# Performance work log

Hardware: AMD Instinct MI355X
Metric: run time of the kernel (lower is better)

The kernel has to match this reference:

```python
import jax, jax.numpy as jnp
import numpy as np

N = 20000; E = 160000; C = 64; SH = 9; NB = 8
S_DIM = 16; MS_HID = 64; FC_HID = 64
RATE = 0.1; LAMBDA = 0.5; R_MAX = 5.0; EV_PER = 16
K = int(RATE * N)          # static master-node count (top-k selection)
E_V = EV_PER * K           # static virtual-edge budget


def _safe_len(vec):
    # smooth norm, safe under autodiff at zero-length edges (self loops)
    return jnp.sqrt(jnp.sum(vec * vec, axis=-1, keepdims=True) + 1e-12)


def _sh(vec):
    # real spherical harmonics lmax=2, 'component' normalization, on unit vectors
    n = vec / _safe_len(vec)
    x, y, z = n[:, 0], n[:, 1], n[:, 2]
    s3 = jnp.sqrt(3.0); s15 = jnp.sqrt(15.0); s5 = jnp.sqrt(5.0)
    return jnp.stack([
        jnp.ones_like(x),
        s3 * x, s3 * y, s3 * z,
        s15 * x * y, s15 * y * z, 0.5 * s5 * (3 * z * z - 1.0),
        s15 * x * z, 0.5 * s15 * (x * x - y * y),
    ], axis=-1)  # [E, 9]


def _bessel(r):
    # Bessel radial basis with p=6 polynomial cutoff envelope; r: [E,1]
    n = jnp.arange(1, NB + 1, dtype=r.dtype)
    b = jnp.sqrt(2.0 / R_MAX) * jnp.sin(n * jnp.pi * r / R_MAX) / jnp.clip(r, 1e-9)
    u = jnp.clip(r / R_MAX, 0.0, 1.0); p = 6.0
    env = 1.0 - (p + 1) * (p + 2) / 2 * u ** p + p * (p + 2) * u ** (p + 1) - p * (p + 1) / 2 * u ** (p + 2)
    return b * env  # [E, NB]


def _conv(h, src, dst, sh, ef, emask, n_nodes, fc_w1, fc_b1, fc_w2, fc_b2, lin_w):
    # TFN-style tensor-product conv: per-edge weights from radial MLP,
    # message = flatten(h[dst] outer sh) * w -> linear -> scatter-mean to src
    w = jax.nn.relu(ef @ fc_w1 + fc_b1) @ fc_w2 + fc_b2            # [E, C*SH]
    tp = (h[dst][:, :, None] * sh[:, None, :]).reshape(sh.shape[0], -1) * w
    msg = (tp @ lin_w) * emask[:, None]                            # [E, C]
    agg = jax.ops.segment_sum(msg, src, num_segments=n_nodes)
    deg = jax.ops.segment_sum(emask, src, num_segments=n_nodes)
    return agg / jnp.clip(deg, 1.0)[:, None]


def setup_inputs() -> dict:
    key = jax.random.key(0)
    ks = jax.random.split(key, 12)
    def lin(k, i, o):
        return (jax.random.normal(k, (i, o), jnp.float32) / np.sqrt(i)).astype(jnp.float32)
    return {
        "h": jax.random.normal(ks[0], (N, C), jnp.float32),
        "pos": jax.random.uniform(ks[1], (N, 3), jnp.float32) * 10.0,
        "edge_index": jax.random.randint(ks[2], (2, E), 0, N, dtype=jnp.int32),
        "fc_w1": lin(ks[3], NB, FC_HID), "fc_b1": jnp.zeros((FC_HID,), jnp.float32),
        "fc_w2": lin(ks[4], FC_HID, C * SH), "fc_b2": jnp.zeros((C * SH,), jnp.float32),
        "lin_w": lin(ks[5], C * SH, C),
        "ms_w1": lin(ks[6], S_DIM, MS_HID), "ms_b1": jnp.zeros((MS_HID,), jnp.float32),
        "ms_w2": lin(ks[7], MS_HID, 1), "ms_b2": jnp.zeros((1,), jnp.float32),
        "vg_wq": lin(ks[8], S_DIM, S_DIM), "vg_wk": lin(ks[9], S_DIM, S_DIM),
    }


def reference(h, pos, fc_w1, fc_b1, fc_w2, fc_b2, lin_w,
              ms_w1, ms_b1, ms_w2, ms_b2, vg_wq, vg_wk, edge_index):
    src, dst = edge_index[0], edge_index[1]
    vec = pos[src] - pos[dst]
    sh = _sh(vec)
    ef = _bessel(_safe_len(vec))
    ones_e = jnp.ones((E,), h.dtype)
    h_update = _conv(h, src, dst, sh, ef, ones_e, N, fc_w1, fc_b1, fc_w2, fc_b2, lin_w)
    h_local = h_update + h  # in_dim == out_dim -> pad is a no-op

    # --- master selection (top-k by learned score; static K) ---
    h_sc = h_local[:, :S_DIM]
    score = jax.nn.sigmoid(
        (jax.nn.relu(h_sc @ ms_w1 + ms_b1) @ ms_w2 + ms_b2).squeeze(-1))  # [N]
    _, top_idx = jax.lax.top_k(score, K)
    node_mask = jnp.zeros((N,), h.dtype).at[top_idx].set(1.0)
    m = score * node_mask
    master_idx = jnp.sort(top_idx)

    # relabel full-graph ids -> master-subgraph ids (masked subgraph extraction)
    node2m = jnp.full((N,), -1, jnp.int32).at[master_idx].set(jnp.arange(K, dtype=jnp.int32))
    src_m, dst_m = node2m[src], node2m[dst]
    e_mask = ((src_m >= 0) & (dst_m >= 0)).astype(h.dtype)
    src_mc = jnp.where(src_m >= 0, src_m, 0)
    dst_mc = jnp.where(dst_m >= 0, dst_m, 0)
    adj = jnp.zeros((K, K), h.dtype).at[src_mc, dst_mc].add(e_mask)

    h_master = h_local[master_idx]
    pos_master = pos[master_idx]
    h_ms = h_master[:, :S_DIM]

    # --- virtual edge generation (attention, thresholded by lambda) ---
    q = h_ms @ vg_wq; kk = h_ms @ vg_wk
    attn = jax.nn.sigmoid(q @ kk.T / np.sqrt(S_DIM))  # [K, K]
    exist = (adj > 0) | jnp.eye(K, dtype=bool)
    A_virtual = jnp.where((~exist) & (attn > LAMBDA), 1.0, 0.0).astype(h.dtype)
    vvals, vidx = jax.lax.top_k((attn * A_virtual).reshape(-1), E_V)
    v_src = (vidx // K).astype(jnp.int32); v_dst = (vidx % K).astype(jnp.int32)
    v_mask = (vvals > 0).astype(h.dtype)

    src_all = jnp.concatenate([src_mc, v_src])
    dst_all = jnp.concatenate([dst_mc, v_dst])
    mask_all = jnp.concatenate([e_mask, v_mask])
    vec_m = pos_master[src_all] - pos_master[dst_all]
    sh_m = _sh(vec_m)
    ef_m = _bessel(_safe_len(vec_m))
    h_m_update = _conv(h_master, src_all, dst_all, sh_m, ef_m, mask_all, K,
                       fc_w1, fc_b1, fc_w2, fc_b2, lin_w)
    h_hier = h_m_update + h_master

    h_hier_exp = jnp.zeros_like(h_local).at[master_idx].set(h_hier)
    m_e = m[:, None]
    h_final = (1.0 - m_e) * h_local + m_e * h_hier_exp
    return (h_final, pos, A_virtual, m)
```

## Files before the change

kernel.cpp:

```cpp
#include <hip/hip_runtime.h>
#include <stdint.h>

constexpr int N_   = 20000;
constexpr int E_   = 160000;
constexpr int C_   = 64;
constexpr int K_   = 2000;
constexpr int EV_  = 32000;
constexpr int EALL_ = E_ + EV_;
constexpr int CSH_ = 576;
constexpr int TB_  = 64;

constexpr size_t OFF_AGG    = 0;
constexpr size_t OFF_DEG    = 5120000;
constexpr size_t OFF_AGGM   = 5200000;
constexpr size_t OFF_DEGM   = 5712000;
constexpr size_t OFF_RANK   = 5720000;
constexpr size_t OFF_MASKA  = 5800000;
constexpr size_t OFF_EXIST  = 6568000;
constexpr size_t OFF_HIST   = 10568000;
constexpr size_t OFF_STATE  = 10572096;
constexpr size_t ZERO_BYTES = 10572352;
constexpr size_t OFF_HLOCAL = 10572352;
constexpr size_t OFF_KEY    = 15692352;
constexpr size_t OFF_SCORE  = 15852352;
constexpr size_t OFF_N2M    = 15932352;
constexpr size_t OFF_MIDX   = 16012352;
constexpr size_t OFF_HM     = 16020352;
constexpr size_t OFF_POSM   = 16532352;
constexpr size_t OFF_Q      = 16556352;
constexpr size_t OFF_KBUF   = 16684352;
constexpr size_t OFF_SRCA   = 16812352;
constexpr size_t OFF_DSTA   = 17580352;
constexpr size_t OFF_TMAX   = 18348352;
constexpr size_t OFF_CAND   = 18410880;

struct RState {
    unsigned long long prefix;
    int R;
    unsigned int cand_count;
    unsigned int sel_count;
    int bin_thresh;
    unsigned int total;
    unsigned int pad;
};

__global__ void k_w0(const float* __restrict__ fc_b1, const float* __restrict__ fc_w2,
                     const float* __restrict__ fc_b2, int* __restrict__ w0nz)
{
    __shared__ float hid0[64];
    __shared__ int nz;
    int tid = threadIdx.x;
    if (tid == 0) nz = 0;
    if (tid < 64) hid0[tid] = fmaxf(fc_b1[tid], 0.0f);
    __syncthreads();
    if (tid < CSH_) {
        float acc = fc_b2[tid];
        for (int k = 0; k < 64; k++) acc += hid0[k] * fc_w2[k * CSH_ + tid];
        if (acc != 0.0f) atomicOr(&nz, 1);
    }
    __syncthreads();
    if (tid == 0) *w0nz = nz;
}

__global__ __launch_bounds__(256) void k_prep(
    int n_edges, const int* __restrict__ src, const int* __restrict__ dst,
    const float* __restrict__ mask, const float* __restrict__ posn,
    const int* __restrict__ w0nz, float* __restrict__ deg,
    float* __restrict__ edata, unsigned int* __restrict__ cnt)
{
    int e = blockIdx.x * 256 + threadIdx.x;
    bool valid = e < n_edges;
    int s_i = 0, d_i = 0; float msk = 0.0f;
    if (valid) {
        msk = mask ? mask[e] : 1.0f;
        if (msk != 0.0f) { s_i = src[e]; d_i = dst[e]; }
    }
    bool active = valid && (msk != 0.0f);

    float vx = 0.f, vy = 0.f, vz = 0.f;
    if (active) {
        vx = posn[s_i*3+0] - posn[d_i*3+0];
        vy = posn[s_i*3+1] - posn[d_i*3+1];
        vz = posn[s_i*3+2] - posn[d_i*3+2];
    }
    float r = sqrtf(vx*vx + vy*vy + vz*vz + 1e-12f);
    float invr = 1.0f / r;
    float x = vx*invr, y = vy*invr, z = vz*invr;
    const float s3 = 1.7320508075688772f, s15 = 3.872983346207417f, s5 = 2.23606797749979f;
    float sh[9];
    sh[0] = 1.0f; sh[1] = s3*x; sh[2] = s3*y; sh[3] = s3*z;
    sh[4] = s15*x*y; sh[5] = s15*y*z; sh[6] = 0.5f*s5*(3.0f*z*z - 1.0f);
    sh[7] = s15*x*z; sh[8] = 0.5f*s15*(x*x - y*y);

    float u = r * 0.2f; u = u > 1.0f ? 1.0f : u;
    float u2 = u*u, u6 = u2*u2*u2, u7 = u6*u, u8 = u7*u;
    float env = 1.0f - 28.0f*u6 + 48.0f*u7 - 21.0f*u8;
    float rc = r > 1e-9f ? r : 1e-9f;
    const float bpref = 0.6324555320336759f;
    const float PIov5 = 0.6283185307179586f;
    float ef[8];
    #pragma unroll
    for (int n = 0; n < 8; n++)
        ef[n] = bpref * sinf(PIov5 * r * (float)(n + 1)) / rc * env;

    if (active) atomicAdd(&deg[s_i], msk);

    bool contrib = active && !((env == 0.0f) && (*w0nz == 0));
    int lane = threadIdx.x & 63;
    unsigned long long b = __ballot(contrib);
    int wc = __popcll(b);
    int base = 0;
    if (lane == 0 && wc) base = (int)atomicAdd(cnt, (unsigned)wc);
    base = __shfl(base, 0);
    if (contrib) {
        int slot = base + __popcll(b & ((1ull << lane) - 1ull));
        float* p = edata + (size_t)slot * 20;
        #pragma unroll
        for (int n = 0; n < 8; n++) p[n] = ef[n];
        #pragma unroll
        for (int t = 0; t < 9; t++) p[8+t] = sh[t];
        p[17] = __int_as_float(s_i);
        p[18] = __int_as_float(d_i);
        p[19] = msk;
    }
}

__global__ __launch_bounds__(256, 3) void k_convg(
    const unsigned int* __restrict__ cnt, const float* __restrict__ edata,
    const float* __restrict__ hn,
    const float* __restrict__ fc_w1, const float* __restrict__ fc_b1,
    const float* __restrict__ fc_w2, const float* __restrict__ fc_b2,
    const float* __restrict__ lin_w, float* __restrict__ agg)
{
    __shared__ float s_misc[TB_ * 12];
    __shared__ __align__(16) float s_hid[64 * 64];
    __shared__ __align__(16) float s_tp[64 * 68];
    __shared__ __align__(16) float s_w[4096];

    const int tid = threadIdx.x;
    const int oq = (tid & 15) * 4;
    const int e0 = (tid >> 4) * 4;

    const int nheavy = (int)*cnt;
    const int nblk = (nheavy + TB_ - 1) / TB_;

    for (int blk = blockIdx.x; blk < nblk; blk += gridDim.x) {
        const int ebase = blk * TB_;
        int nE = nheavy - ebase; if (nE > TB_) nE = TB_;

        __syncthreads();
        for (int idx = tid; idx < TB_ * 12; idx += 256) {
            int e = idx / 12, f = idx - 12 * e;
            float v = 0.0f;
            if (e < nE) {
                const float* p = edata + (size_t)(ebase + e) * 20;
                v = (f < 9) ? p[8 + f] : (f == 9) ? p[17] : (f == 10) ? p[19] : p[18];
            }
            s_misc[idx] = v;
        }
        for (int idx = tid; idx < TB_ * 64; idx += 256) {
            int k = idx >> 6, e = idx & 63;
            float hv = 0.0f;
            if (e < nE) {
                const float* p = edata + (size_t)(ebase + e) * 20;
                float acc = fc_b1[k];
                #pragma unroll
                for (int n = 0; n < 8; n++) acc += p[n] * fc_w1[n * 64 + k];
                hv = fmaxf(acc, 0.0f);
            }
            s_hid[k * 64 + e] = hv;
        }
        float acc[4][4] = {{0,0,0,0},{0,0,0,0},{0,0,0,0},{0,0,0,0}};
        __syncthreads();

        const int d0 = __float_as_int(s_misc[(e0+0) * 12 + 11]);
        const int d1 = __float_as_int(s_misc[(e0+1) * 12 + 11]);
        const int d2 = __float_as_int(s_misc[(e0+2) * 12 + 11]);
        const int d3 = __float_as_int(s_misc[(e0+3) * 12 + 11]);

        for (int cj = 0; cj < 9; cj++) {
            const int j0 = cj * 64;
            if (cj) __syncthreads();
            for (int i4 = tid; i4 < 1024; i4 += 256) {
                int k = i4 >> 4, q4 = (i4 & 15) * 4;
                *reinterpret_cast<float4*>(&s_w[k * 64 + q4]) =
                    *reinterpret_cast<const float4*>(&fc_w2[k * CSH_ + j0 + q4]);
            }
            __syncthreads();

            const int jb = j0 + oq;
            const int c0 = jb / 9, c1 = (jb + 3) / 9;
            float hA0 = hn[d0 * 64 + c0], hB0 = hn[d0 * 64 + c1];
            float hA1 = hn[d1 * 64 + c0], hB1 = hn[d1 * 64 + c1];
            float hA2 = hn[d2 * 64 + c0], hB2 = hn[d2 * 64 + c1];
            float hA3 = hn[d3 * 64 + c0], hB3 = hn[d3 * 64 + c1];

            float a[4][4];
            #pragma unroll
            for (int q = 0; q < 4; q++) {
                float b = fc_b2[jb + q];
                a[0][q]=b; a[1][q]=b; a[2][q]=b; a[3][q]=b;
            }
            #pragma unroll 4
            for (int k = 0; k < 64; k++) {
                float4 w4 = *reinterpret_cast<const float4*>(&s_w[k * 64 + oq]);
                float4 h4 = *reinterpret_cast<const float4*>(&s_hid[k * 64 + e0]);
                a[0][0]+=h4.x*w4.x; a[0][1]+=h4.x*w4.y; a[0][2]+=h4.x*w4.z; a[0][3]+=h4.x*w4.w;
                a[1][0]+=h4.y*w4.x; a[1][1]+=h4.y*w4.y; a[1][2]+=h4.y*w4.z; a[1][3]+=h4.y*w4.w;
                a[2][0]+=h4.z*w4.x; a[2][1]+=h4.z*w4.y; a[2][2]+=h4.z*w4.z; a[2][3]+=h4.z*w4.w;
                a[3][0]+=h4.w*w4.x; a[3][1]+=h4.w*w4.y; a[3][2]+=h4.w*w4.z; a[3][3]+=h4.w*w4.w;
            }
            #pragma unroll
            for (int q = 0; q < 4; q++) {
                int j = jb + q; int cc = j / 9; int si = j - 9 * cc;
                float4 tpv;
                tpv.x = (cc == c0 ? hA0 : hB0) * s_misc[(e0+0) * 12 + si] * a[0][q];
                tpv.y = (cc == c0 ? hA1 : hB1) * s_misc[(e0+1) * 12 + si] * a[1][q];
                tpv.z = (cc == c0 ? hA2 : hB2) * s_misc[(e0+2) * 12 + si] * a[2][q];
                tpv.w = (cc == c0 ? hA3 : hB3) * s_misc[(e0+3) * 12 + si] * a[3][q];
                *reinterpret_cast<float4*>(&s_tp[(oq + q) * 68 + e0]) = tpv;
            }
            __syncthreads();

            for (int i4 = tid; i4 < 1024; i4 += 256) {
                *reinterpret_cast<float4*>(&s_w[i4 * 4]) =
                    *reinterpret_cast<const float4*>(&lin_w[j0 * 64 + i4 * 4]);
            }
            __syncthreads();

            #pragma unroll 4
            for (int jj = 0; jj < 64; jj++) {
                float4 l4 = *reinterpret_cast<const float4*>(&s_w[jj * 64 + oq]);
                float4 t4 = *reinterpret_cast<const float4*>(&s_tp[jj * 68 + e0]);
                acc[0][0]+=t4.x*l4.x; acc[0][1]+=t4.x*l4.y; acc[0][2]+=t4.x*l4.z; acc[0][3]+=t4.x*l4.w;
                acc[1][0]+=t4.y*l4.x; acc[1][1]+=t4.y*l4.y; acc[1][2]+=t4.y*l4.z; acc[1][3]+=t4.y*l4.w;
                acc[2][0]+=t4.z*l4.x; acc[2][1]+=t4.z*l4.y; acc[2][2]+=t4.z*l4.z; acc[2][3]+=t4.z*l4.w;
                acc[3][0]+=t4.w*l4.x; acc[3][1]+=t4.w*l4.y; acc[3][2]+=t4.w*l4.z; acc[3][3]+=t4.w*l4.w;
            }
        }

        #pragma unroll
        for (int t = 0; t < 4; t++) {
            float mk = s_misc[(e0+t) * 12 + 10];
            if (mk != 0.0f) {
                int s = __float_as_int(s_misc[(e0+t) * 12 + 9]);
                #pragma unroll
                for (int q = 0; q < 4; q++) atomicAdd(&agg[s * 64 + oq + q], acc[t][q] * mk);
            }
        }
    }
}

__global__ __launch_bounds__(256) void k_hlscore(const float* __restrict__ h,
    const float* __restrict__ agg, const float* __restrict__ deg,
    const float* __restrict__ ms_w1, const float* __restrict__ ms_b1,
    const float* __restrict__ ms_w2, const float* __restrict__ ms_b2,
    float* __restrict__ h_local, float* __restrict__ score, unsigned long long* __restrict__ key)
{
    int wid = threadIdx.x >> 6, lane = threadIdx.x & 63;
    int n = blockIdx.x * 4 + wid;
    if (n >= N_) return;
    float d = fmaxf(deg[n], 1.0f);
    float hl = h[n*64 + lane] + agg[n*64 + lane] / d;
    h_local[n*64 + lane] = hl;
    float acc = ms_b1[lane];
    #pragma unroll
    for (int i = 0; i < 16; i++) acc += __shfl(hl, i) * ms_w1[i*64 + lane];
    acc = fmaxf(acc, 0.0f);
    float part = acc * ms_w2[lane];
    #pragma unroll
    for (int off = 32; off > 0; off >>= 1) part += __shfl_xor(part, off);
    if (lane == 0) {
        float s = part + ms_b2[0];
        float sc = 1.0f / (1.0f + expf(-s));
        score[n] = sc;
        key[n] = ((unsigned long long)__float_as_uint(sc) << 32)
               | (unsigned long long)(0xFFFFFFFFu - (unsigned)n);
    }
}

__global__ __launch_bounds__(256) void k_rank(const unsigned long long* __restrict__ key,
                                              int* __restrict__ rankcnt)
{
    int i = blockIdx.x * 256 + threadIdx.x;
    int seg = blockIdx.y;
    int lo = seg * 1250, hi = lo + 1250;
    unsigned long long my = (i < N_) ? key[i] : ~0ull;
    int cnt = 0;
    #pragma unroll 8
    for (int j = lo; j < hi; j++) cnt += (key[j] > my) ? 1 : 0;
    if (i < N_ && cnt) atomicAdd(&rankcnt[i], cnt);
}

__global__ __launch_bounds__(1024) void k_scanfin(const int* __restrict__ rankcnt,
    const float* __restrict__ score, int* __restrict__ node2m, int* __restrict__ midx,
    float* __restrict__ m_out)
{
    __shared__ int wsum[16];
    __shared__ int wbase[16];
    __shared__ int s_base;
    int tid = threadIdx.x, lane = tid & 63, wv = tid >> 6;
    if (tid == 0) s_base = 0;
    __syncthreads();
    for (int c = 0; c < 20; c++) {
        int idx = c * 1024 + tid;
        int sel = 0;
        if (idx < N_) {
            sel = (rankcnt[idx] < K_) ? 1 : 0;
            m_out[idx] = sel ? score[idx] : 0.0f;
        }
        int v = sel;
        #pragma unroll
        for (int off = 1; off < 64; off <<= 1) {
            int u = __shfl_up(v, off);
            if (lane >= off) v += u;
        }
        if (lane == 63) wsum[wv] = v;
        __syncthreads();
        if (tid == 0) {
            int runb = s_base;
            for (int w = 0; w < 16; w++) { wbase[w] = runb; runb += wsum[w]; }
            s_base = runb;
        }
        __syncthreads();
        if (idx < N_) {
            if (sel) { int rk = wbase[wv] + v - 1; node2m[idx] = rk; midx[rk] = idx; }
            else node2m[idx] = -1;
        }
    }
}

__global__ __launch_bounds__(256) void k_mastex(const int* __restrict__ midx,
    const float* __restrict__ h_local, const float* __restrict__ pos,
    const float* __restrict__ vg_wq, const float* __restrict__ vg_wk,
    const int* __restrict__ src, const int* __restrict__ dst, const int* __restrict__ node2m,
    float* __restrict__ h_m, float* __restrict__ pos_m,
    float* __restrict__ qbuf, float* __restrict__ kbuf,
    int* __restrict__ src_all, int* __restrict__ dst_all,
    float* __restrict__ mask_all, unsigned char* __restrict__ exist)
{
    int b = blockIdx.x;
    if (b < 500) {
        int mi = b * 4 + (threadIdx.x >> 6);
        int lane = threadIdx.x & 63;
        int node = midx[mi];
        h_m[mi*64 + lane] = h_local[node*64 + lane];
        if (lane < 3) pos_m[mi*3 + lane] = pos[node*3 + lane];
        if (lane < 32) {
            int j = lane & 15;
            const float* wm = (lane < 16) ? vg_wq : vg_wk;
            float acc = 0.0f;
            #pragma unroll
            for (int i = 0; i < 16; i++) acc += h_local[node*64 + i] * wm[i*16 + j];
            if (lane < 16) qbuf[mi*16 + j] = acc; else kbuf[mi*16 + j] = acc;
        }
    } else {
        int e = (b - 500) * 256 + threadIdx.x;
        int sm = node2m[src[e]], dm = node2m[dst[e]];
        bool em = (sm >= 0) && (dm >= 0);
        int smc = sm >= 0 ? sm : 0;
        int dmc = dm >= 0 ? dm : 0;
        src_all[e] = smc; dst_all[e] = dmc; mask_all[e] = em ? 1.0f : 0.0f;
        if (em) exist[smc * K_ + dmc] = 1;
    }
}

constexpr int NTILE_ = (K_ / 16) * (K_ / 16);
__global__ __launch_bounds__(256) void k_attn1(const float* __restrict__ qbuf,
    const float* __restrict__ kbuf, const unsigned char* __restrict__ exist,
    float* __restrict__ Av, float* __restrict__ tmax, unsigned int* __restrict__ hist,
    RState* st, unsigned int* __restrict__ done_ctr)
{
    constexpr int TBK = K_ / 16;
    __shared__ float sq[16][17], sk[16][17];
    __shared__ unsigned int lh[1024];
    __shared__ float wmax[4];
    __shared__ unsigned int ha[1024], hb[1024];
    __shared__ unsigned int s_last;
    int tid = threadIdx.x;
    for (int b = tid; b < 1024; b += 256) lh[b] = 0;

    for (int t = blockIdx.x; t < NTILE_; t += gridDim.x) {
        int bi = t / TBK, bj = t % TBK;
        int i0 = bi * 16, j0 = bj * 16;
        int r = tid >> 4, c = tid & 15;
        __syncthreads();
        sq[r][c] = qbuf[(i0 + r) * 16 + c];
        sk[r][c] = kbuf[(j0 + r) * 16 + c];
        __syncthreads();
        int ti = tid >> 4, tj = tid & 15;
        float dot = 0.0f;
        #pragma unroll
        for (int cc = 0; cc < 16; cc++) dot += sq[ti][cc] * sk[tj][cc];
        float attn = 1.0f / (1.0f + expf(-dot * 0.25f));
        int gi = i0 + ti, gj = j0 + tj;
        int flat = gi * K_ + gj;
        bool ex = (exist[flat] != 0) || (gi == gj);
        bool av = (!ex) && (attn > 0.5f);
        Av[flat] = av ? 1.0f : 0.0f;
        float cv = av ? attn : 0.0f;
        if (av) {
            unsigned bin = (__float_as_uint(attn) - 0x3F000000u) >> 13;
            if (bin > 1023u) bin = 1023u;
            atomicAdd(&lh[bin], 1u);
        }
        float wm = cv;
        #pragma unroll
        for (int off = 32; off > 0; off >>= 1) wm = fmaxf(wm, __shfl_xor(wm, off));
        int wid = tid >> 6, lane = tid & 63;
        if (lane == 0) wmax[wid] = wm;
        __syncthreads();
        if (tid == 0) tmax[t] = fmaxf(fmaxf(wmax[0], wmax[1]), fmaxf(wmax[2], wmax[3]));
    }
    __syncthreads();
    for (int b = tid; b < 1024; b += 256) {
        unsigned v = lh[b];
        if (v) atomicAdd(&hist[b], v);
    }
    __syncthreads();
    __threadfence();
    if (tid == 0) s_last = (atomicAdd(done_ctr, 1u) == (unsigned)gridDim.x - 1u) ? 1u : 0u;
    __syncthreads();
    if (!s_last) return;
    __threadfence();
    for (int b = tid; b < 1024; b += 256) ha[b] = hist[b];
    __syncthreads();
    unsigned* srcp = ha; unsigned* dstp = hb;
    for (int off = 1; off < 1024; off <<= 1) {
        for (int b = tid; b < 1024; b += 256)
            dstp[b] = srcp[b] + ((b + off < 1024) ? srcp[b + off] : 0u);
        __syncthreads();
        unsigned* tmp = srcp; srcp = dstp; dstp = tmp;
    }
    unsigned total = srcp[0];
    int R = (total < (unsigned)EV_) ? (int)total : EV_;
    if (tid == 0) {
        st->R = R; st->total = total; st->cand_count = 0; st->sel_count = 0;
        if (R == 0) st->bin_thresh = 1024;
    }
    __syncthreads();
    if (R > 0) {
        for (int b = tid; b < 1024; b += 256) {
            unsigned hi2 = (b == 1023) ? 0u : srcp[b + 1];
            if ((int)srcp[b] >= R && (int)hi2 < R) st->bin_thresh = b;
        }
    }
}

__global__ __launch_bounds__(256) void k_attn2(const float* __restrict__ qbuf,
    const float* __restrict__ kbuf, const unsigned char* __restrict__ exist,
    const float* __restrict__ tmax, RState* st, unsigned long long* __restrict__ cand)
{
    constexpr int TBK = K_ / 16;
    __shared__ float sq[16][17], sk[16][17];
    __shared__ int wb[4];
    __shared__ int bb;
    int tid = threadIdx.x;
    unsigned tbits = 0x3F000000u + ((unsigned)st->bin_thresh << 13);

    for (int t = blockIdx.x; t < NTILE_; t += gridDim.x) {
        if (__float_as_uint(tmax[t]) < tbits) continue;
        int bi = t / TBK, bj = t % TBK;
        int i0 = bi * 16, j0 = bj * 16;
        int r = tid >> 4, c = tid & 15;
        __syncthreads();
        sq[r][c] = qbuf[(i0 + r) * 16 + c];
        sk[r][c] = kbuf[(j0 + r) * 16 + c];
        __syncthreads();
        int ti = tid >> 4, tj = tid & 15;
        float dot = 0.0f;
        #pragma unroll
        for (int cc = 0; cc < 16; cc++) dot += sq[ti][cc] * sk[tj][cc];
        float attn = 1.0f / (1.0f + expf(-dot * 0.25f));
        int gi = i0 + ti, gj = j0 + tj;
        int flat = gi * K_ + gj;
        bool ex = (exist[flat] != 0) || (gi == gj);
        bool store = (!ex) && (attn > 0.5f) && (__float_as_uint(attn) >= tbits);

        unsigned long long keyv = ((unsigned long long)__float_as_uint(attn) << 32)
                                | (unsigned long long)(0xFFFFFFFFu - (unsigned)flat);
        int wid = tid >> 6, lane = tid & 63;
        unsigned long long b = __ballot(store);
        int wc = __popcll(b);
        if (lane == 0) wb[wid] = wc;
        __syncthreads();
        if (tid == 0) {
            int s = 0;
            for (int w = 0; w < 4; w++) { int cc2 = wb[w]; wb[w] = s; s += cc2; }
            bb = s ? (int)atomicAdd(&st->cand_count, (unsigned)s) : 0;
        }
        __syncthreads();
        if (store) {
            int slot = bb + wb[wid] + __popcll(b & ((1ull << lane) - 1ull));
            cand[slot] = keyv;
        }
    }
}

__global__ __launch_bounds__(1024) void k_radixsel(RState* st,
    const unsigned long long* __restrict__ cand,
    int* __restrict__ src_all, int* __restrict__ dst_all, float* __restrict__ mask_all)
{
    __shared__ unsigned int lh[256];
    __shared__ unsigned int suf[256];
    __shared__ unsigned int s_tie[8192];
    __shared__ unsigned int s_pref, s_R, s_tiecnt, s_cfth;
    int tid = threadIdx.x;
    int n = (int)st->cand_count;
    int R = st->R;
    if (tid == 0) { s_pref = 0x3F000000u; s_R = (unsigned)R; s_tiecnt = 0; s_cfth = 0; }
    __syncthreads();

    unsigned long long T;
    if (R > 0) {
        for (int p = 0; p < 3; p++) {
            if (tid < 256) lh[tid] = 0;
            __syncthreads();
            unsigned pref = s_pref;
            int sh_d = 16 - 8 * p;
            unsigned pm = 0xFFFFFFFFu << (sh_d + 8);
            for (int i = tid; i < n; i += 1024) {
                unsigned a = (unsigned)(cand[i] >> 32);
                if ((a & pm) == (pref & pm))
                    atomicAdd(&lh[(a >> sh_d) & 255u], 1u);
            }
            __syncthreads();
            if (tid < 256) suf[tid] = lh[tid];
            __syncthreads();
            for (int off = 1; off < 256; off <<= 1) {
                unsigned v = 0;
                if (tid < 256 && tid + off < 256) v = suf[tid + off];
                __syncthreads();
                if (tid < 256) suf[tid] += v;
                __syncthreads();
            }
            if (tid < 256) {
                unsigned Rc = s_R;
                unsigned hi2 = (tid == 255) ? 0u : suf[tid + 1];
                if (suf[tid] >= Rc && hi2 < Rc) {
                    s_pref = pref | ((unsigned)tid << sh_d);
                    s_R = Rc - hi2;
                }
            }
            __syncthreads();
        }
        unsigned Ta = s_pref;
        unsigned Rrem = s_R;
        for (int i = tid; i < n; i += 1024) {
            unsigned long long kv = cand[i];
            if ((unsigned)(kv >> 32) == Ta) {
                unsigned pos = atomicAdd(&s_tiecnt, 1u);
                if (pos < 8192u) s_tie[pos] = (unsigned)(kv & 0xFFFFFFFFull);
            }
        }
        __syncthreads();
        unsigned Cq = s_tiecnt; if (Cq > 8192u) Cq = 8192u;
        if (Rrem >= 1u && Rrem < Cq) {
            for (int i = tid; i < (int)Cq; i += 1024) {
                unsigned me = s_tie[i];
                unsigned r = 0;
                for (int j = 0; j < (int)Cq; j++) r += (s_tie[j] > me) ? 1u : 0u;
                if (r == Rrem - 1u) s_cfth = me;
            }
        }
        __syncthreads();
        T = ((unsigned long long)Ta << 32) | (unsigned long long)s_cfth;
    } else {
        T = ~0ull;
    }

    int lane = tid & 63;
    for (int i0 = 0; i0 < n; i0 += 1024) {
        int i = i0 + tid;
        bool sel = (i < n) && (cand[i] >= T);
        unsigned long long b = __ballot(sel);
        int wc = __popcll(b);
        int basep = 0;
        if (lane == 0 && wc) basep = (int)atomicAdd(&st->sel_count, (unsigned)wc);
        basep = __shfl(basep, 0);
        if (sel) {
            int slot = basep + __popcll(b & ((1ull << lane) - 1ull));
            if (slot < EV_) {
                unsigned flat = 0xFFFFFFFFu - (unsigned)(cand[i] & 0xFFFFFFFFull);
                src_all[E_ + slot] = (int)(flat / (unsigned)K_);
                dst_all[E_ + slot] = (int)(flat % (unsigned)K_);
                mask_all[E_ + slot] = 1.0f;
            }
        }
    }
}

__global__ void k_finalpos(const float* __restrict__ h_local, const int* __restrict__ node2m,
    const float* __restrict__ aggm, const float* __restrict__ degm, const float* __restrict__ h_m,
    const float* __restrict__ m_out, const float* __restrict__ pos,
    float* __restrict__ out_h, float* __restrict__ out_pos)
{
    int idx = blockIdx.x * 256 + threadIdx.x;
    if (idx < N_ * 3) out_pos[idx] = pos[idx];
    if (idx >= N_ * C_) return;
    int i = idx >> 6, c = idx & 63;
    float mval = m_out[i];
    int mi = node2m[i];
    float hh = 0.0f;
    if (mi >= 0) hh = aggm[mi*64 + c] / fmaxf(degm[mi], 1.0f) + h_m[mi*64 + c];
    out_h[idx] = (1.0f - mval) * h_local[idx] + mval * hh;
}

extern "C" void kernel_launch(void* const* d_in, const int* in_sizes, int n_in,
                              void* d_out, int out_size, void* d_ws, size_t ws_size,
                              hipStream_t stream)
{
    (void)in_sizes; (void)n_in; (void)out_size; (void)ws_size;
    const float* h     = (const float*)d_in[0];
    const float* pos   = (const float*)d_in[1];
    const int*   eidx  = (const int*)d_in[2];
    const float* fc_w1 = (const float*)d_in[3];
    const float* fc_b1 = (const float*)d_in[4];
    const float* fc_w2 = (const float*)d_in[5];
    const float* fc_b2 = (const float*)d_in[6];
    const float* lin_w = (const float*)d_in[7];
    const float* ms_w1 = (const float*)d_in[8];
    const float* ms_b1 = (const float*)d_in[9];
    const float* ms_w2 = (const float*)d_in[10];
    const float* ms_b2 = (const float*)d_in[11];
    const float* vg_wq = (const float*)d_in[12];
    const float* vg_wk = (const float*)d_in[13];

    char* ws = (char*)d_ws;
    float* agg     = (float*)(ws + OFF_AGG);
    float* deg     = (float*)(ws + OFF_DEG);
    float* aggm    = (float*)(ws + OFF_AGGM);
    float* degm    = (float*)(ws + OFF_DEGM);
    int*   rankcnt = (int*)(ws + OFF_RANK);
    float* mask_all = (float*)(ws + OFF_MASKA);
    unsigned char* exist = (unsigned char*)(ws + OFF_EXIST);
    unsigned int* hist = (unsigned int*)(ws + OFF_HIST);
    RState* st     = (RState*)(ws + OFF_STATE);
    unsigned int* cnt0 = (unsigned int*)(ws + OFF_STATE + 64);
    unsigned int* cnt1 = (unsigned int*)(ws + OFF_STATE + 68);
    int*   w0nz    = (int*)(ws + OFF_STATE + 72);
    unsigned int* done_a1 = (unsigned int*)(ws + OFF_STATE + 76);
    float* h_local = (float*)(ws + OFF_HLOCAL);
    unsigned long long* key = (unsigned long long*)(ws + OFF_KEY);
    float* score   = (float*)(ws + OFF_SCORE);
    int*   node2m  = (int*)(ws + OFF_N2M);
    int*   midx    = (int*)(ws + OFF_MIDX);
    float* h_m     = (float*)(ws + OFF_HM);
    float* pos_m   = (float*)(ws + OFF_POSM);
    float* qbuf    = (float*)(ws + OFF_Q);
    float* kbuf    = (float*)(ws + OFF_KBUF);
    int*   src_all = (int*)(ws + OFF_SRCA);
    int*   dst_all = (int*)(ws + OFF_DSTA);
    float* tmax    = (float*)(ws + OFF_TMAX);
    unsigned long long* cand = (unsigned long long*)(ws + OFF_CAND);
    float* edata   = (float*)(ws + OFF_CAND);

    float* out_h   = (float*)d_out;
    float* out_pos = out_h + (size_t)N_ * C_;
    float* out_av  = out_pos + (size_t)N_ * 3;
    float* out_m   = out_av + (size_t)K_ * K_;

    hipMemsetAsync(ws, 0, ZERO_BYTES, stream);

    k_w0<<<1, 576, 0, stream>>>(fc_b1, fc_w2, fc_b2, w0nz);

    k_prep<<<E_ / 256, 256, 0, stream>>>(E_, eidx, eidx + E_, nullptr, pos, w0nz, deg, edata, cnt0);
    k_convg<<<768, 256, 0, stream>>>(cnt0, edata, h, fc_w1, fc_b1, fc_w2, fc_b2, lin_w, agg);

    k_hlscore<<<(N_ + 3) / 4, 256, 0, stream>>>(h, agg, deg, ms_w1, ms_b1, ms_w2, ms_b2,
                                                h_local, score, key);

    k_rank<<<dim3((N_ + 255) / 256, 16), 256, 0, stream>>>(key, rankcnt);
    k_scanfin<<<1, 1024, 0, stream>>>(rankcnt, score, node2m, midx, out_m);

    k_mastex<<<500 + E_ / 256, 256, 0, stream>>>(midx, h_local, pos, vg_wq, vg_wk,
        eidx, eidx + E_, node2m, h_m, pos_m, qbuf, kbuf, src_all, dst_all, mask_all, exist);

    k_attn1<<<1024, 256, 0, stream>>>(qbuf, kbuf, exist, out_av, tmax, hist, st, done_a1);
    k_attn2<<<1024, 256, 0, stream>>>(qbuf, kbuf, exist, tmax, st, cand);
    k_radixsel<<<1, 1024, 0, stream>>>(st, cand, src_all, dst_all, mask_all);

    k_prep<<<EALL_ / 256, 256, 0, stream>>>(EALL_, src_all, dst_all, mask_all, pos_m, w0nz,
                                            degm, edata, cnt1);
    k_convg<<<768, 256, 0, stream>>>(cnt1, edata, h_m, fc_w1, fc_b1, fc_w2, fc_b2, lin_w, aggm);

    k_finalpos<<<(N_ * C_ + 255) / 256, 256, 0, stream>>>(h_local, node2m, aggm, degm, h_m,
                                                          out_m, pos, out_h, out_pos);
}
```

Measured before the change: 737.8 us.

## Fuse workspace zeroing into init kernel and merge rank with scan via last-block

```diff
diff --git a/kernel.cpp b/kernel.cpp
--- a/kernel.cpp
+++ b/kernel.cpp
@@ -19,7 +19,6 @@
 constexpr size_t OFF_EXIST  = 6568000;
 constexpr size_t OFF_HIST   = 10568000;
 constexpr size_t OFF_STATE  = 10572096;
-constexpr size_t ZERO_BYTES = 10572352;
 constexpr size_t OFF_HLOCAL = 10572352;
 constexpr size_t OFF_KEY    = 15692352;
 constexpr size_t OFF_SCORE  = 15852352;
@@ -44,22 +43,30 @@
     unsigned int pad;
 };
 
-__global__ void k_w0(const float* __restrict__ fc_b1, const float* __restrict__ fc_w2,
-                     const float* __restrict__ fc_b2, int* __restrict__ w0nz)
-{
-    __shared__ float hid0[64];
-    __shared__ int nz;
-    int tid = threadIdx.x;
-    if (tid == 0) nz = 0;
-    if (tid < 64) hid0[tid] = fmaxf(fc_b1[tid], 0.0f);
-    __syncthreads();
-    if (tid < CSH_) {
-        float acc = fc_b2[tid];
-        for (int k = 0; k < 64; k++) acc += hid0[k] * fc_w2[k * CSH_ + tid];
-        if (acc != 0.0f) atomicOr(&nz, 1);
-    }
-    __syncthreads();
-    if (tid == 0) *w0nz = nz;
+__global__ __launch_bounds__(256) void k_init(const float* __restrict__ fc_b1,
+    const float* __restrict__ fc_w2, const float* __restrict__ fc_b2, char* __restrict__ ws)
+{
+    float4 zero4 = make_float4(0.f, 0.f, 0.f, 0.f);
+    float4* z = (float4*)ws;
+    int nz4 = (int)(OFF_STATE / 16);
+    for (int i = blockIdx.x * 256 + threadIdx.x; i < nz4; i += gridDim.x * 256) z[i] = zero4;
+    if (blockIdx.x == gridDim.x - 1) {
+        __shared__ float hid0[64];
+        __shared__ int nz;
+        int t = threadIdx.x;
+        float4* zs = (float4*)(ws + OFF_STATE);
+        if (t < 16) zs[t] = zero4;
+        if (t == 0) nz = 0;
+        if (t < 64) hid0[t] = fmaxf(fc_b1[t], 0.0f);
+        __syncthreads();
+        for (int j = t; j < CSH_; j += 256) {
+            float acc = fc_b2[j];
+            for (int k = 0; k < 64; k++) acc += hid0[k] * fc_w2[k * CSH_ + j];
+            if (acc != 0.0f) atomicOr(&nz, 1);
+        }
+        __syncthreads();
+        if (t == 0) *(int*)(ws + OFF_STATE + 72) = nz;
+    }
 }
 
 __global__ __launch_bounds__(256) void k_prep(
@@ -279,52 +286,63 @@
     }
 }
 
-__global__ __launch_bounds__(256) void k_rank(const unsigned long long* __restrict__ key,
-                                              int* __restrict__ rankcnt)
-{
-    int i = blockIdx.x * 256 + threadIdx.x;
-    int seg = blockIdx.y;
-    int lo = seg * 1250, hi = lo + 1250;
-    unsigned long long my = (i < N_) ? key[i] : ~0ull;
-    int cnt = 0;
-    #pragma unroll 8
-    for (int j = lo; j < hi; j++) cnt += (key[j] > my) ? 1 : 0;
-    if (i < N_ && cnt) atomicAdd(&rankcnt[i], cnt);
-}
-
-__global__ __launch_bounds__(1024) void k_scanfin(const int* __restrict__ rankcnt,
-    const float* __restrict__ score, int* __restrict__ node2m, int* __restrict__ midx,
-    float* __restrict__ m_out)
-{
-    __shared__ int wsum[16];
-    __shared__ int wbase[16];
-    __shared__ int s_base;
+__global__ __launch_bounds__(256) void k_rankscan(const unsigned long long* __restrict__ key,
+    int* __restrict__ rankcnt, const float* __restrict__ score,
+    int* __restrict__ node2m, int* __restrict__ midx, float* __restrict__ m_out,
+    unsigned int* __restrict__ done)
+{
     int tid = threadIdx.x, lane = tid & 63, wv = tid >> 6;
-    if (tid == 0) s_base = 0;
-    __syncthreads();
-    for (int c = 0; c < 20; c++) {
-        int idx = c * 1024 + tid;
-        int sel = 0;
+    {
+        int ib = blockIdx.x % 79;
+        int seg = blockIdx.x / 79;
+        int i = ib * 256 + tid;
+        int lo = seg * 1250, hi = lo + 1250;
+        unsigned long long my = (i < N_) ? key[i] : ~0ull;
+        int cnt = 0;
+        #pragma unroll 8
+        for (int j = lo; j < hi; j++) cnt += (key[j] > my) ? 1 : 0;
+        if (i < N_ && cnt) atomicAdd(&rankcnt[i], cnt);
+    }
+    __threadfence();
+    __syncthreads();
+    __shared__ unsigned int s_last;
+    if (tid == 0) s_last = (atomicAdd(done, 1u) == (unsigned)gridDim.x - 1u) ? 1u : 0u;
+    __syncthreads();
+    if (!s_last) return;
+    __threadfence();
+
+    const int base = tid * 79;
+    unsigned long long m0 = 0ull; unsigned m1 = 0u;
+    int csel = 0;
+    for (int k = 0; k < 79; k++) {
+        int idx = base + k;
         if (idx < N_) {
-            sel = (rankcnt[idx] < K_) ? 1 : 0;
+            int r = atomicAdd(&rankcnt[idx], 0);
+            int sel = (r < K_) ? 1 : 0;
             m_out[idx] = sel ? score[idx] : 0.0f;
-        }
-        int v = sel;
-        #pragma unroll
-        for (int off = 1; off < 64; off <<= 1) {
-            int u = __shfl_up(v, off);
-            if (lane >= off) v += u;
-        }
-        if (lane == 63) wsum[wv] = v;
-        __syncthreads();
-        if (tid == 0) {
-            int runb = s_base;
-            for (int w = 0; w < 16; w++) { wbase[w] = runb; runb += wsum[w]; }
-            s_base = runb;
-        }
-        __syncthreads();
+            if (sel) {
+                if (k < 64) m0 |= (1ull << k); else m1 |= (1u << (k - 64));
+                csel++;
+            }
+        }
+    }
+    __shared__ int wsum[4], wbase[4];
+    int v = csel;
+    #pragma unroll
+    for (int off = 1; off < 64; off <<= 1) {
+        int u = __shfl_up(v, off);
+        if (lane >= off) v += u;
+    }
+    if (lane == 63) wsum[wv] = v;
+    __syncthreads();
+    if (tid == 0) { int run = 0; for (int w = 0; w < 4; w++) { int c = wsum[w]; wbase[w] = run; run += c; } }
+    __syncthreads();
+    int run = wbase[wv] + v - csel;
+    for (int k = 0; k < 79; k++) {
+        int idx = base + k;
         if (idx < N_) {
-            if (sel) { int rk = wbase[wv] + v - 1; node2m[idx] = rk; midx[rk] = idx; }
+            bool sel = (k < 64) ? ((m0 >> k) & 1ull) : ((m1 >> (k - 64)) & 1u);
+            if (sel) { node2m[idx] = run; midx[run] = idx; run++; }
             else node2m[idx] = -1;
         }
     }
@@ -423,7 +441,7 @@
     __syncthreads();
     if (!s_last) return;
     __threadfence();
-    for (int b = tid; b < 1024; b += 256) ha[b] = hist[b];
+    for (int b = tid; b < 1024; b += 256) ha[b] = atomicAdd(&hist[b], 0u);
     __syncthreads();
     unsigned* srcp = ha; unsigned* dstp = hb;
     for (int off = 1; off < 1024; off <<= 1) {
@@ -640,6 +658,7 @@
     unsigned int* cnt1 = (unsigned int*)(ws + OFF_STATE + 68);
     int*   w0nz    = (int*)(ws + OFF_STATE + 72);
     unsigned int* done_a1 = (unsigned int*)(ws + OFF_STATE + 76);
+    unsigned int* done_rk = (unsigned int*)(ws + OFF_STATE + 80);
     float* h_local = (float*)(ws + OFF_HLOCAL);
     unsigned long long* key = (unsigned long long*)(ws + OFF_KEY);
     float* score   = (float*)(ws + OFF_SCORE);
@@ -660,9 +679,7 @@
     float* out_av  = out_pos + (size_t)N_ * 3;
     float* out_m   = out_av + (size_t)K_ * K_;
 
-    hipMemsetAsync(ws, 0, ZERO_BYTES, stream);
-
-    k_w0<<<1, 576, 0, stream>>>(fc_b1, fc_w2, fc_b2, w0nz);
+    k_init<<<768, 256, 0, stream>>>(fc_b1, fc_w2, fc_b2, ws);
 
     k_prep<<<E_ / 256, 256, 0, stream>>>(E_, eidx, eidx + E_, nullptr, pos, w0nz, deg, edata, cnt0);
     k_convg<<<768, 256, 0, stream>>>(cnt0, edata, h, fc_w1, fc_b1, fc_w2, fc_b2, lin_w, agg);
@@ -670,14 +687,13 @@
     k_hlscore<<<(N_ + 3) / 4, 256, 0, stream>>>(h, agg, deg, ms_w1, ms_b1, ms_w2, ms_b2,
                                                 h_local, score, key);
 
-    k_rank<<<dim3((N_ + 255) / 256, 16), 256, 0, stream>>>(key, rankcnt);
-    k_scanfin<<<1, 1024, 0, stream>>>(rankcnt, score, node2m, midx, out_m);
+    k_rankscan<<<79 * 16, 256, 0, stream>>>(key, rankcnt, score, node2m, midx, out_m, done_rk);
 
     k_mastex<<<500 + E_ / 256, 256, 0, stream>>>(midx, h_local, pos, vg_wq, vg_wk,
         eidx, eidx + E_, node2m, h_m, pos_m, qbuf, kbuf, src_all, dst_all, mask_all, exist);
 
-    k_attn1<<<1024, 256, 0, stream>>>(qbuf, kbuf, exist, out_av, tmax, hist, st, done_a1);
-    k_attn2<<<1024, 256, 0, stream>>>(qbuf, kbuf, exist, tmax, st, cand);
+    k_attn1<<<2048, 256, 0, stream>>>(qbuf, kbuf, exist, out_av, tmax, hist, st, done_a1);
+    k_attn2<<<2048, 256, 0, stream>>>(qbuf, kbuf, exist, tmax, st, cand);
     k_radixsel<<<1, 1024, 0, stream>>>(st, cand, src_all, dst_all, mask_all);
 
     k_prep<<<EALL_ / 256, 256, 0, stream>>>(EALL_, src_all, dst_all, mask_all, pos_m, w0nz,
```

Result: slower. 963.5 us (+30.6%).
